# Optimization experiments

Measured on AMD Instinct MI355X. Metric: run time of the kernel, lower is better.

## Reference

```python
import math
import jax, jax.numpy as jnp
import numpy as np


def _alibi_slopes(n):
    def pow2_slopes(n):
        start = 2.0 ** (-(2.0 ** (-(math.log2(n) - 3))))
        return [start * (start ** i) for i in range(n)]
    if math.log2(n).is_integer():
        return pow2_slopes(n)
    cp2 = 2 ** math.floor(math.log2(n))
    return pow2_slopes(cp2) + _alibi_slopes(2 * cp2)[0::2][: n - cp2]


NUM_HEADS = 16


def setup_inputs() -> dict:
    key = jax.random.key(0)
    ks = jax.random.split(key, 5)
    B, S, H = 2, 2048, 2048
    return {
        "hidden_states": jax.random.normal(ks[0], (B, S, H), jnp.float32),
        "w_qkv": jax.random.normal(ks[1], (H, 3 * H), jnp.float32) * (H ** -0.5),
        "b_qkv": jax.random.normal(ks[2], (3 * H,), jnp.float32) * 0.02,
        "w_proj": jax.random.normal(ks[3], (H, H), jnp.float32) * (H ** -0.5),
        "b_proj": jax.random.normal(ks[4], (H,), jnp.float32) * 0.02,
    }


def reference(hidden_states, w_qkv, b_qkv, w_proj, b_proj):
    B, S, H = hidden_states.shape
    nh = NUM_HEADS
    hd = H // nh
    scale = 1.0 / hd  # mup scale_qk_dot_by_d=True -> d^-1 (not d^-0.5)

    qkv = hidden_states @ w_qkv + b_qkv  # [B,S,3H]
    q, k, v = jnp.split(qkv, 3, axis=-1)
    q = q.reshape(B, S, nh, hd)
    k = k.reshape(B, S, nh, hd)
    v = v.reshape(B, S, nh, hd)

    scores = jnp.einsum("bqhd,bkhd->bhqk", q, k) * scale  # [B,nh,S,S]

    slopes = jnp.asarray(_alibi_slopes(nh), dtype=scores.dtype)  # [nh]
    pos = jnp.arange(S)
    rel = (pos[None, :] - pos[:, None]).astype(scores.dtype)  # j - i, <=0 in causal region
    bias = slopes[:, None, None] * rel[None, :, :]  # [nh,S,S]
    causal = pos[None, :] <= pos[:, None]  # [S,S]

    scores = jnp.where(causal[None, None], scores + bias[None], jnp.finfo(scores.dtype).min)
    attn = jax.nn.softmax(scores, axis=-1)

    out = jnp.einsum("bhqk,bkhd->bqhd", attn, v).reshape(B, S, H)
    return out @ w_proj + b_proj
```

## Files before the change

### kernel.cpp

```cpp
#include <hip/hip_runtime.h>
#include <hip/hip_bf16.h>

typedef short bf16x8 __attribute__((ext_vector_type(8)));
typedef float f32x4 __attribute__((ext_vector_type(4)));
typedef unsigned short ushort_t;

#define NH 16
#define HD 128
#define SEQ 2048
#define HID 2048
#define NQKV 6144
#define BATCH 2

__device__ __forceinline__ ushort_t f2bf(float x) {
    unsigned u = __builtin_bit_cast(unsigned, x);
    u = (u + 0x7fffu + ((u >> 16) & 1u)) >> 16;
    return (ushort_t)u;
}

__device__ __forceinline__ void gl2lds16(const ushort_t* g, ushort_t* l) {
    __builtin_amdgcn_global_load_lds(
        (__attribute__((address_space(1))) void*)(g),
        (__attribute__((address_space(3))) void*)(l), 16, 0, 0);
}

__global__ __launch_bounds__(256) void prep_fused(
    const float* __restrict__ hidden, ushort_t* __restrict__ hbf,
    const float* __restrict__ wqkv, ushort_t* __restrict__ wqkvT,
    const float* __restrict__ wproj, ushort_t* __restrict__ wprojT) {
    const int bid = blockIdx.x;
    const int t = threadIdx.x;
    if (bid >= 12288 && bid < 16384) {
        int i = (bid - 12288) * 256 + t;
        float4 a0 = *(const float4*)(hidden + (size_t)i * 8);
        float4 a1 = *(const float4*)(hidden + (size_t)i * 8 + 4);
        union { ushort_t u[8]; uint4 v; } p;
        p.u[0]=f2bf(a0.x); p.u[1]=f2bf(a0.y); p.u[2]=f2bf(a0.z); p.u[3]=f2bf(a0.w);
        p.u[4]=f2bf(a1.x); p.u[5]=f2bf(a1.y); p.u[6]=f2bf(a1.z); p.u[7]=f2bf(a1.w);
        *(uint4*)(hbf + (size_t)i * 8) = p.v;
        return;
    }
    const float* w;
    ushort_t* wT;
    int N, bx, by;
    if (bid < 12288) {
        w = wqkv; wT = wqkvT; N = NQKV;
        bx = bid % 192; by = bid / 192;
    } else {
        int b2 = bid - 16384;
        w = wproj; wT = wprojT; N = HID;
        bx = b2 % 64; by = b2 / 64;
    }
    __shared__ float tile[32][33];
    const int nb = bx * 32, kb = by * 32;
    const int tx = t & 31, ty = t >> 5;
#pragma unroll
    for (int i = 0; i < 4; ++i) {
        int k = kb + ty + i * 8;
        tile[ty + i * 8][tx] = w[(size_t)k * N + nb + tx];
    }
    __syncthreads();
#pragma unroll
    for (int i = 0; i < 4; ++i) {
        int n = nb + ty + i * 8;
        wT[(size_t)n * HID + kb + tx] = f2bf(tile[tx][ty + i * 8]);
    }
}

#define GEMM_KLOOP(A_, BT_)                                                     \
    const int t = threadIdx.x;                                                  \
    const int w = t >> 6, lane = t & 63, lm = lane & 15, lq = lane >> 4;        \
    const int wm = (w >> 1) * 64, wn = (w & 1) * 64;                            \
    const int lrow = lane >> 3, lsw = (lane & 7) ^ lrow;                        \
    f32x4 acc[4][4] = {};                                                       \
    const ushort_t* gA = A_ + (size_t)(mb + w * 32 + lrow) * HID + lsw * 8;     \
    const ushort_t* gB = BT_ + (size_t)(nb + w * 32 + lrow) * HID + lsw * 8;    \
    for (int kb = 0; kb < HID; kb += 64) {                                      \
        __syncthreads();                                                        \
        _Pragma("unroll")                                                       \
        for (int c = 0; c < 4; ++c) {                                           \
            gl2lds16(gA + (size_t)c * 8 * HID + kb, At + (w * 256 + c * 64) * 8); \
            gl2lds16(gB + (size_t)c * 8 * HID + kb, Bt + (w * 256 + c * 64) * 8); \
        }                                                                       \
        __syncthreads();                                                        \
        _Pragma("unroll")                                                       \
        for (int kc = 0; kc < 2; ++kc) {                                        \
            const int slot = (kc * 4 + lq) ^ (lm & 7);                          \
            bf16x8 af[4], bfr[4];                                               \
            _Pragma("unroll")                                                   \
            for (int mt = 0; mt < 4; ++mt)                                      \
                af[mt] = ((const bf16x8*)At)[(wm + mt * 16 + lm) * 8 + slot];   \
            _Pragma("unroll")                                                   \
            for (int nt = 0; nt < 4; ++nt)                                      \
                bfr[nt] = ((const bf16x8*)Bt)[(wn + nt * 16 + lm) * 8 + slot];  \
            _Pragma("unroll")                                                   \
            for (int mt = 0; mt < 4; ++mt)                                      \
                _Pragma("unroll")                                               \
                for (int nt = 0; nt < 4; ++nt)                                  \
                    acc[mt][nt] = __builtin_amdgcn_mfma_f32_16x16x32_bf16(      \
                        af[mt], bfr[nt], acc[mt][nt], 0, 0, 0);                 \
        }                                                                       \
    }

__global__ __launch_bounds__(256) void gemm_qkv(
    const ushort_t* __restrict__ A, const ushort_t* __restrict__ BT,
    const float* __restrict__ bias,
    ushort_t* __restrict__ qbuf, ushort_t* __restrict__ kbuf,
    ushort_t* __restrict__ vTbuf) {
    __shared__ unsigned shbuf[128 * 68];
    ushort_t* At = (ushort_t*)shbuf;
    ushort_t* Bt = At + 128 * 64;
    const int mb = blockIdx.x * 128;
    const int nb = blockIdx.y * 128;
    GEMM_KLOOP(A, BT)

    const int sec = nb >> 11;
    if (sec < 2) {
#pragma unroll
        for (int mt = 0; mt < 4; ++mt)
#pragma unroll
            for (int nt = 0; nt < 4; ++nt)
#pragma unroll
                for (int r = 0; r < 4; ++r) {
                    int m = mb + wm + mt * 16 + lq * 4 + r;
                    int c = nb + wn + nt * 16 + lm;
                    float val = acc[mt][nt][r] + bias[c];
                    int h = (c >> 7) & 15;
                    int d = c & 127;
                    int b = m >> 11, s = m & 2047;
                    size_t bh = (size_t)(b * NH + h);
                    ushort_t* dst = (sec == 0) ? qbuf : kbuf;
                    dst[(bh * SEQ + s) * HD + d] = f2bf(val);
                }
    } else {
        __syncthreads();
        unsigned* T = shbuf;
#pragma unroll
        for (int mt = 0; mt < 4; ++mt)
#pragma unroll
            for (int nt = 0; nt < 4; ++nt) {
                const int cl = wn + nt * 16 + lm;
                const int ml = wm + mt * 16 + lq * 4;
                const float bb = bias[nb + cl];
#pragma unroll
                for (int r = 0; r < 4; r += 2) {
                    unsigned pk = (unsigned)f2bf(acc[mt][nt][r] + bb) |
                                  ((unsigned)f2bf(acc[mt][nt][r + 1] + bb) << 16);
                    T[cl * 68 + ((ml + r) >> 1)] = pk;
                }
            }
        __syncthreads();
        const int d = t & 127, sh = t >> 7;
        const int b = mb >> 11, sbase = mb & 2047;
        const int hv = (nb >> 7) - 32;
        ushort_t* vrow = vTbuf + ((size_t)(b * NH + hv) * HD + d) * SEQ + sbase + sh * 64;
#pragma unroll
        for (int i = 0; i < 8; ++i)
            *(uint4*)(vrow + i * 8) = *(const uint4*)&T[d * 68 + sh * 32 + i * 4];
    }
}

__global__ __launch_bounds__(256) void gemm_proj(
    const ushort_t* __restrict__ A, const ushort_t* __restrict__ BT,
    const float* __restrict__ bias, float* __restrict__ out) {
    __shared__ ushort_t Abuf[128 * 64];
    __shared__ ushort_t Bbuf[128 * 64];
    ushort_t* At = Abuf;
    ushort_t* Bt = Bbuf;
    const int mb = blockIdx.x * 128;
    const int nb = blockIdx.y * 128;
    GEMM_KLOOP(A, BT)
#pragma unroll
    for (int mt = 0; mt < 4; ++mt)
#pragma unroll
        for (int nt = 0; nt < 4; ++nt)
#pragma unroll
            for (int r = 0; r < 4; ++r) {
                int m = mb + wm + mt * 16 + lq * 4 + r;
                int c = nb + wn + nt * 16 + lm;
                out[(size_t)m * HID + c] = acc[mt][nt][r] + bias[c];
            }
}

__global__ __launch_bounds__(256) void attn_kernel(
    const ushort_t* __restrict__ qb, const ushort_t* __restrict__ kbuf,
    const ushort_t* __restrict__ vT, ushort_t* __restrict__ ob) {
    __shared__ ushort_t Ks[2][64 * 128];
    __shared__ ushort_t Vs[2][128 * 64];
    __shared__ ushort_t Ps[4][16 * 72];

    const int bid = blockIdx.x;
    const int x = bid & 7, g = bid >> 3;
    const int qt = 31 - (g >> 2);
    const int bh = ((g & 3) << 3) | x;
    const int qbase = qt * 64;
    const int t = threadIdx.x, w = t >> 6, lane = t & 63;
    const int lm = lane & 15, lq = lane >> 4;

    const ushort_t* Qg = qb + (size_t)bh * SEQ * HD;
    const ushort_t* Kg = kbuf + (size_t)bh * SEQ * HD;
    const ushort_t* Vg = vT + (size_t)bh * HD * SEQ;

    const float LOG2E = 1.44269504f;
    const int h = bh & 15;
    const float slope2 = exp2f(-0.5f * (float)(h + 1)) * LOG2E;
    const float scale2 = (1.0f / 128.0f) * LOG2E;

    const int qg = qbase + w * 16 + lm;

    bf16x8 qf[4];
#pragma unroll
    for (int kc = 0; kc < 4; ++kc) {
        uint4 qv = *(const uint4*)(Qg + (size_t)qg * HD + kc * 32 + lq * 8);
        qf[kc] = __builtin_bit_cast(bf16x8, qv);
    }

    float foff[4][4];
#pragma unroll
    for (int mt = 0; mt < 4; ++mt)
#pragma unroll
        for (int r = 0; r < 4; ++r)
            foff[mt][r] = slope2 * (float)(mt * 16 + lq * 4 + r);

    int koffs[4], voffs[4];
#pragma unroll
    for (int i = 0; i < 4; ++i) {
        int ci = i * 256 + t;
        int kr = ci >> 4, ks = ci & 15;
        int kcg = (ks & 8) | ((ks & 7) ^ (kr & 7));
        koffs[i] = kr * HD + kcg * 8;
        int vr = ci >> 3, vs = ci & 7;
        int vcg = vs ^ (vr & 7);
        voffs[i] = vr * SEQ + vcg * 8;
    }

#define ATTN_STAGE(KT, BUF)                                                   \
    {                                                                         \
        const ushort_t* Kt_ = Kg + (size_t)(KT) * 64 * HD;                    \
        const ushort_t* Vt_ = Vg + (size_t)(KT) * 64;                         \
        _Pragma("unroll")                                                     \
        for (int i = 0; i < 4; ++i) {                                         \
            gl2lds16(Kt_ + koffs[i], Ks[BUF] + (i * 256 + w * 64) * 8);       \
            gl2lds16(Vt_ + voffs[i], Vs[BUF] + (i * 256 + w * 64) * 8);       \
        }                                                                     \
    }

    float mrow = -1e30f, lrow = 0.0f;
    f32x4 O[8] = {};
    const int nkt = qt + 1;

    ATTN_STAGE(0, 0)
    __syncthreads();

    for (int kt = 0; kt < nkt; ++kt) {
        const int cur = kt & 1;
        if (kt + 1 < nkt) ATTN_STAGE(kt + 1, cur ^ 1)

        f32x4 sacc[4] = {};
        __builtin_amdgcn_s_setprio(1);
#pragma unroll
        for (int kc = 0; kc < 4; ++kc) {
            const int slot = ((kc * 4 + lq) & 8) | (((kc * 4 + lq) & 7) ^ (lm & 7));
#pragma unroll
            for (int mt = 0; mt < 4; ++mt) {
                bf16x8 bk = *(const bf16x8*)&Ks[cur][((mt * 16 + lm) * 16 + slot) * 8];
                sacc[mt] = __builtin_amdgcn_mfma_f32_16x16x32_bf16(bk, qf[kc], sacc[mt], 0, 0, 0);
            }
        }
        __builtin_amdgcn_s_setprio(0);

        const float sbase = slope2 * (float)(kt * 64 - qg);
        float sc[4][4];
        if (kt == qt) {
#pragma unroll
            for (int mt = 0; mt < 4; ++mt)
#pragma unroll
                for (int r = 0; r < 4; ++r) {
                    float s = sacc[mt][r] * scale2 + (sbase + foff[mt][r]);
                    sc[mt][r] = (kt * 64 + mt * 16 + lq * 4 + r <= qg) ? s : -3e38f;
                }
        } else {
#pragma unroll
            for (int mt = 0; mt < 4; ++mt)
#pragma unroll
                for (int r = 0; r < 4; ++r)
                    sc[mt][r] = sacc[mt][r] * scale2 + (sbase + foff[mt][r]);
        }

        float tm = sc[0][0];
#pragma unroll
        for (int mt = 0; mt < 4; ++mt)
#pragma unroll
            for (int r = 0; r < 4; ++r) tm = fmaxf(tm, sc[mt][r]);
        tm = fmaxf(tm, __shfl_xor(tm, 16));
        tm = fmaxf(tm, __shfl_xor(tm, 32));

        const bool noresc = __all(tm <= mrow + 8.0f) && (kt > 0);
        float mnew, alpha;
        if (noresc) {
            mnew = mrow;
            alpha = 1.0f;
        } else {
            mnew = fmaxf(mrow, tm);
            alpha = __builtin_amdgcn_exp2f(mrow - mnew);
        }
        mrow = mnew;

        float psum = 0.0f;
#pragma unroll
        for (int mt = 0; mt < 4; ++mt) {
            float p0 = __builtin_amdgcn_exp2f(sc[mt][0] - mnew);
            float p1 = __builtin_amdgcn_exp2f(sc[mt][1] - mnew);
            float p2 = __builtin_amdgcn_exp2f(sc[mt][2] - mnew);
            float p3 = __builtin_amdgcn_exp2f(sc[mt][3] - mnew);
            psum += (p0 + p1) + (p2 + p3);
            uint2 wv;
            wv.x = ((unsigned)f2bf(p1) << 16) | f2bf(p0);
            wv.y = ((unsigned)f2bf(p3) << 16) | f2bf(p2);
            *(uint2*)&Ps[w][lm * 72 + mt * 16 + lq * 4] = wv;
        }
        psum += __shfl_xor(psum, 16);
        psum += __shfl_xor(psum, 32);
        lrow = lrow * alpha + psum;

        if (!noresc) {
            float av[4];
#pragma unroll
            for (int r = 0; r < 4; ++r) av[r] = __shfl(alpha, lq * 4 + r);
#pragma unroll
            for (int nt = 0; nt < 8; ++nt)
#pragma unroll
                for (int r = 0; r < 4; ++r) O[nt][r] *= av[r];
        }

        asm volatile("s_waitcnt lgkmcnt(0)" ::: "memory");
        __builtin_amdgcn_s_setprio(1);
#pragma unroll
        for (int kc2 = 0; kc2 < 2; ++kc2) {
            bf16x8 ap = *(const bf16x8*)&Ps[w][lm * 72 + kc2 * 32 + lq * 8];
            const int slot = (kc2 * 4 + lq) ^ (lm & 7);
#pragma unroll
            for (int nt = 0; nt < 8; ++nt) {
                bf16x8 bv = *(const bf16x8*)&Vs[cur][((nt * 16 + lm) * 8 + slot) * 8];
                O[nt] = __builtin_amdgcn_mfma_f32_16x16x32_bf16(ap, bv, O[nt], 0, 0, 0);
            }
        }
        __builtin_amdgcn_s_setprio(0);

        __syncthreads();
    }

    float lb[4];
#pragma unroll
    for (int r = 0; r < 4; ++r)
        lb[r] = __builtin_amdgcn_rcpf(__shfl(lrow, lq * 4 + r));
    const int b = bh >> 4;
#pragma unroll
    for (int nt = 0; nt < 8; ++nt)
#pragma unroll
        for (int r = 0; r < 4; ++r) {
            int s = qbase + w * 16 + lq * 4 + r;
            int d = nt * 16 + lm;
            ob[((size_t)(b * SEQ + s)) * HID + h * HD + d] = f2bf(O[nt][r] * lb[r]);
        }
#undef ATTN_STAGE
}

extern "C" void kernel_launch(void* const* d_in, const int* in_sizes, int n_in,
                              void* d_out, int out_size, void* d_ws, size_t ws_size,
                              hipStream_t stream) {
    const float* hidden = (const float*)d_in[0];
    const float* w_qkv = (const float*)d_in[1];
    const float* b_qkv = (const float*)d_in[2];
    const float* w_proj = (const float*)d_in[3];
    const float* b_proj = (const float*)d_in[4];
    float* out = (float*)d_out;

    char* ws = (char*)d_ws;
    size_t off = 0;
    ushort_t* wqkvT = (ushort_t*)(ws + off); off += (size_t)NQKV * HID * 2;
    ushort_t* wprojT = (ushort_t*)(ws + off); off += (size_t)HID * HID * 2;
    ushort_t* hbf = (ushort_t*)(ws + off); off += (size_t)BATCH * SEQ * HID * 2;
    ushort_t* qw = (ushort_t*)(ws + off); off += (size_t)BATCH * NH * SEQ * HD * 2;
    ushort_t* kw = (ushort_t*)(ws + off); off += (size_t)BATCH * NH * SEQ * HD * 2;
    ushort_t* vTw = (ushort_t*)(ws + off); off += (size_t)BATCH * NH * SEQ * HD * 2;
    ushort_t* attnw = (ushort_t*)(ws + off); off += (size_t)BATCH * SEQ * HID * 2;

    prep_fused<<<dim3(20480), 256, 0, stream>>>(
        hidden, hbf, w_qkv, wqkvT, w_proj, wprojT);

    gemm_qkv<<<dim3(BATCH * SEQ / 128, NQKV / 128), 256, 0, stream>>>(
        hbf, wqkvT, b_qkv, qw, kw, vTw);

    attn_kernel<<<dim3(BATCH * NH * 32), 256, 0, stream>>>(qw, kw, vTw, attnw);

    gemm_proj<<<dim3(BATCH * SEQ / 128, HID / 128), 256, 0, stream>>>(
        attnw, wprojT, b_proj, out);
}
```

Baseline: 365.6 us.

## Rework QKV GEMM into 256x128 tiles with multi-stage LDS pipeline and enlarge attention blocks

The QKV GEMM now runs 512-thread blocks over 256x128 output tiles. It uses a hand-scheduled four-phase K loop that prefetches several half-tiles ahead into swizzled LDS, with explicit barriers, waitcnts and priority hints meant to overlap global loads with MFMA work. The attention kernel moves to 512 threads covering 128 query rows per block, so each K/V tile is shared by twice as many waves. In exchange it drops double buffering for a single buffer with two barriers per iteration, and waves past their diagonal skip compute but still join the loads and barriers. Losing load/compute overlap in attention and the idle diagonal waves could offset the gain from larger tiles.

```diff
diff --git a/kernel.cpp b/kernel.cpp
--- a/kernel.cpp
+++ b/kernel.cpp
@@ -102,61 +102,141 @@
         }                                                                       \
     }
 
-__global__ __launch_bounds__(256) void gemm_qkv(
+#define QSTAGE_A(SBUF, SKH, STILE)                                            \
+    _Pragma("unroll")                                                         \
+    for (int j = 0; j < 2; ++j)                                               \
+        gl2lds16(gA + soffA[j] + (STILE) * 64 + (SKH) * 32,                   \
+                 lds + ((SBUF) * 2 + (SKH)) * 8192 + (j * 512 + w * 64) * 8);
+
+#define QSTAGE_B(SBUF, SKH, STILE)                                            \
+    gl2lds16(gB + soffB + (STILE) * 64 + (SKH) * 32,                          \
+             lds + 32768 + ((SBUF) * 2 + (SKH)) * 4096 + (w * 64) * 8);
+
+#define QPHASE4(BUF, KH, SBUF, SKH, STILE, DRAIN)                             \
+    QSTAGE_A(SBUF, SKH, STILE)                                                \
+    QSTAGE_B(SBUF, SKH, STILE)                                                \
+    _Pragma("unroll")                                                         \
+    for (int mf = 0; mf < 4; ++mf) {                                          \
+        int rr = wm + mf * 16 + lm;                                           \
+        int slot = rr * 4 + (lq ^ ((rr >> 1) & 3));                           \
+        af[mf] = *(const bf16x8*)&lds[((BUF) * 2 + (KH)) * 8192 + slot * 8];  \
+    }                                                                         \
+    _Pragma("unroll")                                                         \
+    for (int nf = 0; nf < 4; ++nf) {                                          \
+        int rr = wn + nf * 16 + lm;                                           \
+        int slot = rr * 4 + (lq ^ ((rr >> 1) & 3));                           \
+        bfr[nf] = *(const bf16x8*)&lds[32768 + ((BUF) * 2 + (KH)) * 4096 + slot * 8]; \
+    }                                                                         \
+    asm volatile("" ::: "memory");                                            \
+    __builtin_amdgcn_s_barrier();                                             \
+    __builtin_amdgcn_sched_barrier(0);                                        \
+    __builtin_amdgcn_s_setprio(1);                                            \
+    _Pragma("unroll")                                                         \
+    for (int mf = 0; mf < 4; ++mf)                                            \
+        _Pragma("unroll")                                                     \
+        for (int nf = 0; nf < 4; ++nf)                                        \
+            acc[mf][nf] = __builtin_amdgcn_mfma_f32_16x16x32_bf16(            \
+                af[mf], bfr[nf], acc[mf][nf], 0, 0, 0);                       \
+    __builtin_amdgcn_s_setprio(0);                                            \
+    __builtin_amdgcn_sched_barrier(0);                                        \
+    if (DRAIN) { asm volatile("s_waitcnt vmcnt(3)" ::: "memory"); }           \
+    asm volatile("" ::: "memory");                                            \
+    __builtin_amdgcn_s_barrier();
+
+__global__ __launch_bounds__(512) void gemm_qkv(
     const ushort_t* __restrict__ A, const ushort_t* __restrict__ BT,
     const float* __restrict__ bias,
     ushort_t* __restrict__ qbuf, ushort_t* __restrict__ kbuf,
     ushort_t* __restrict__ vTbuf) {
-    __shared__ unsigned shbuf[128 * 68];
-    ushort_t* At = (ushort_t*)shbuf;
-    ushort_t* Bt = At + 128 * 64;
-    const int mb = blockIdx.x * 128;
-    const int nb = blockIdx.y * 128;
-    GEMM_KLOOP(A, BT)
+    __shared__ ushort_t lds[49152];
+    const int t = threadIdx.x;
+    const int w = t >> 6, lane = t & 63, lm = lane & 15, lq = lane >> 4;
+    const int wm = (w >> 1) * 64, wn = (w & 1) * 64;
+    const int mb = blockIdx.x * 256, nb = blockIdx.y * 128;
+
+    const ushort_t* gA = A + (size_t)mb * HID;
+    const ushort_t* gB = BT + (size_t)nb * HID;
+
+    int soffA[2];
+#pragma unroll
+    for (int j = 0; j < 2; ++j) {
+        int r = j * 128 + (t >> 2);
+        int c = (t & 3) ^ ((r >> 1) & 3);
+        soffA[j] = r * HID + c * 8;
+    }
+    int soffB;
+    {
+        int r = t >> 2;
+        int c = (t & 3) ^ ((r >> 1) & 3);
+        soffB = r * HID + c * 8;
+    }
+
+    f32x4 acc[4][4] = {};
+    bf16x8 af[4], bfr[4];
+
+    QSTAGE_A(0, 0, 0) QSTAGE_B(0, 0, 0)
+    QSTAGE_A(0, 1, 0) QSTAGE_B(0, 1, 0)
+    QSTAGE_A(1, 0, 1) QSTAGE_B(1, 0, 1)
+    asm volatile("s_waitcnt vmcnt(0)" ::: "memory");
+    __builtin_amdgcn_s_barrier();
+
+#pragma unroll 1
+    for (int i = 0; i < 16; ++i) {
+        const int Tb = 2 * i + 1;
+        const int T2 = (2 * i + 2) & 31, T3 = (2 * i + 3) & 31;
+        QPHASE4(0, 0, 1, 1, Tb, 0)
+        QPHASE4(0, 1, 0, 0, T2, 1)
+        QPHASE4(1, 0, 0, 1, T2, 0)
+        QPHASE4(1, 1, 1, 0, T3, 1)
+    }
+
+    asm volatile("s_waitcnt vmcnt(0)" ::: "memory");
 
     const int sec = nb >> 11;
     if (sec < 2) {
 #pragma unroll
-        for (int mt = 0; mt < 4; ++mt)
-#pragma unroll
-            for (int nt = 0; nt < 4; ++nt)
+        for (int mf = 0; mf < 4; ++mf)
+#pragma unroll
+            for (int nf = 0; nf < 4; ++nf)
 #pragma unroll
                 for (int r = 0; r < 4; ++r) {
-                    int m = mb + wm + mt * 16 + lq * 4 + r;
-                    int c = nb + wn + nt * 16 + lm;
-                    float val = acc[mt][nt][r] + bias[c];
-                    int h = (c >> 7) & 15;
+                    int m = mb + wm + mf * 16 + lq * 4 + r;
+                    int c = nb + wn + nf * 16 + lm;
+                    float val = acc[mf][nf][r] + bias[c];
+                    int hh = (c >> 7) & 15;
                     int d = c & 127;
                     int b = m >> 11, s = m & 2047;
-                    size_t bh = (size_t)(b * NH + h);
+                    size_t bh = (size_t)(b * NH + hh);
                     ushort_t* dst = (sec == 0) ? qbuf : kbuf;
                     dst[(bh * SEQ + s) * HD + d] = f2bf(val);
                 }
     } else {
         __syncthreads();
-        unsigned* T = shbuf;
-#pragma unroll
-        for (int mt = 0; mt < 4; ++mt)
-#pragma unroll
-            for (int nt = 0; nt < 4; ++nt) {
-                const int cl = wn + nt * 16 + lm;
-                const int ml = wm + mt * 16 + lq * 4;
-                const float bb = bias[nb + cl];
+        unsigned* T = (unsigned*)lds;
+        const int b = mb >> 11, sbase = mb & 2047;
+        const int hv = (nb >> 7) - 32;
+#pragma unroll
+        for (int nf = 0; nf < 4; ++nf) {
+            const int clc = wn + nf * 16 + lm;
+            const float bb = bias[nb + clc];
+#pragma unroll
+            for (int mf = 0; mf < 4; ++mf) {
+                const int ml = wm + mf * 16 + lq * 4;
 #pragma unroll
                 for (int r = 0; r < 4; r += 2) {
-                    unsigned pk = (unsigned)f2bf(acc[mt][nt][r] + bb) |
-                                  ((unsigned)f2bf(acc[mt][nt][r + 1] + bb) << 16);
-                    T[cl * 68 + ((ml + r) >> 1)] = pk;
+                    unsigned pk = (unsigned)f2bf(acc[mf][nf][r] + bb) |
+                                  ((unsigned)f2bf(acc[mf][nf][r + 1] + bb) << 16);
+                    T[clc * 132 + ((ml + r) >> 1)] = pk;
                 }
             }
+        }
         __syncthreads();
-        const int d = t & 127, sh = t >> 7;
-        const int b = mb >> 11, sbase = mb & 2047;
-        const int hv = (nb >> 7) - 32;
-        ushort_t* vrow = vTbuf + ((size_t)(b * NH + hv) * HD + d) * SEQ + sbase + sh * 64;
-#pragma unroll
-        for (int i = 0; i < 8; ++i)
-            *(uint4*)(vrow + i * 8) = *(const uint4*)&T[d * 68 + sh * 32 + i * 4];
+        const int dd = t & 127, sh = t >> 7;
+        ushort_t* vrow = vTbuf +
+            ((size_t)(b * NH + hv) * HD + dd) * SEQ + sbase + sh * 64;
+#pragma unroll
+        for (int ii = 0; ii < 8; ++ii)
+            *(uint4*)(vrow + ii * 8) = *(const uint4*)&T[dd * 132 + sh * 32 + ii * 4];
     }
 }
 
@@ -182,18 +262,18 @@
             }
 }
 
-__global__ __launch_bounds__(256) void attn_kernel(
+__global__ __launch_bounds__(512) void attn_kernel(
     const ushort_t* __restrict__ qb, const ushort_t* __restrict__ kbuf,
     const ushort_t* __restrict__ vT, ushort_t* __restrict__ ob) {
-    __shared__ ushort_t Ks[2][64 * 128];
-    __shared__ ushort_t Vs[2][128 * 64];
-    __shared__ ushort_t Ps[4][16 * 72];
+    __shared__ ushort_t Ks[64 * 128];
+    __shared__ ushort_t Vs[128 * 64];
+    __shared__ ushort_t Ps[8][16 * 72];
 
     const int bid = blockIdx.x;
     const int x = bid & 7, g = bid >> 3;
-    const int qt = 31 - (g >> 2);
+    const int qt = 15 - (g >> 2);
     const int bh = ((g & 3) << 3) | x;
-    const int qbase = qt * 64;
+    const int qbase = qt * 128;
     const int t = threadIdx.x, w = t >> 6, lane = t & 63;
     const int lm = lane & 15, lq = lane >> 4;
 
@@ -207,6 +287,7 @@
     const float scale2 = (1.0f / 128.0f) * LOG2E;
 
     const int qg = qbase + w * 16 + lm;
+    const int ktd = (qbase + w * 16) >> 6;
 
     bf16x8 qf[4];
 #pragma unroll
@@ -222,10 +303,10 @@
         for (int r = 0; r < 4; ++r)
             foff[mt][r] = slope2 * (float)(mt * 16 + lq * 4 + r);
 
-    int koffs[4], voffs[4];
-#pragma unroll
-    for (int i = 0; i < 4; ++i) {
-        int ci = i * 256 + t;
+    int koffs[2], voffs[2];
+#pragma unroll
+    for (int i = 0; i < 2; ++i) {
+        int ci = i * 512 + t;
         int kr = ci >> 4, ks = ci & 15;
         int kcg = (ks & 8) | ((ks & 7) ^ (kr & 7));
         koffs[i] = kr * HD + kcg * 8;
@@ -234,27 +315,24 @@
         voffs[i] = vr * SEQ + vcg * 8;
     }
 
-#define ATTN_STAGE(KT, BUF)                                                   \
-    {                                                                         \
-        const ushort_t* Kt_ = Kg + (size_t)(KT) * 64 * HD;                    \
-        const ushort_t* Vt_ = Vg + (size_t)(KT) * 64;                         \
-        _Pragma("unroll")                                                     \
-        for (int i = 0; i < 4; ++i) {                                         \
-            gl2lds16(Kt_ + koffs[i], Ks[BUF] + (i * 256 + w * 64) * 8);       \
-            gl2lds16(Vt_ + voffs[i], Vs[BUF] + (i * 256 + w * 64) * 8);       \
-        }                                                                     \
-    }
-
     float mrow = -1e30f, lrow = 0.0f;
     f32x4 O[8] = {};
-    const int nkt = qt + 1;
-
-    ATTN_STAGE(0, 0)
-    __syncthreads();
+    const int nkt = 2 * qt + 2;
 
     for (int kt = 0; kt < nkt; ++kt) {
-        const int cur = kt & 1;
-        if (kt + 1 < nkt) ATTN_STAGE(kt + 1, cur ^ 1)
+        __syncthreads();
+        {
+            const ushort_t* Kt_ = Kg + (size_t)kt * 64 * HD;
+            const ushort_t* Vt_ = Vg + (size_t)kt * 64;
+#pragma unroll
+            for (int i = 0; i < 2; ++i) {
+                gl2lds16(Kt_ + koffs[i], Ks + (i * 512 + w * 64) * 8);
+                gl2lds16(Vt_ + voffs[i], Vs + (i * 512 + w * 64) * 8);
+            }
+        }
+        __syncthreads();
+
+        if (kt > ktd) continue;
 
         f32x4 sacc[4] = {};
         __builtin_amdgcn_s_setprio(1);
@@ -263,7 +341,7 @@
             const int slot = ((kc * 4 + lq) & 8) | (((kc * 4 + lq) & 7) ^ (lm & 7));
 #pragma unroll
             for (int mt = 0; mt < 4; ++mt) {
-                bf16x8 bk = *(const bf16x8*)&Ks[cur][((mt * 16 + lm) * 16 + slot) * 8];
+                bf16x8 bk = *(const bf16x8*)&Ks[((mt * 16 + lm) * 16 + slot) * 8];
                 sacc[mt] = __builtin_amdgcn_mfma_f32_16x16x32_bf16(bk, qf[kc], sacc[mt], 0, 0, 0);
             }
         }
@@ -271,7 +349,7 @@
 
         const float sbase = slope2 * (float)(kt * 64 - qg);
         float sc[4][4];
-        if (kt == qt) {
+        if (kt == ktd) {
 #pragma unroll
             for (int mt = 0; mt < 4; ++mt)
 #pragma unroll
@@ -341,13 +419,11 @@
             const int slot = (kc2 * 4 + lq) ^ (lm & 7);
 #pragma unroll
             for (int nt = 0; nt < 8; ++nt) {
-                bf16x8 bv = *(const bf16x8*)&Vs[cur][((nt * 16 + lm) * 8 + slot) * 8];
+                bf16x8 bv = *(const bf16x8*)&Vs[((nt * 16 + lm) * 8 + slot) * 8];
                 O[nt] = __builtin_amdgcn_mfma_f32_16x16x32_bf16(ap, bv, O[nt], 0, 0, 0);
             }
         }
         __builtin_amdgcn_s_setprio(0);
-
-        __syncthreads();
     }
 
     float lb[4];
@@ -363,7 +439,6 @@
             int d = nt * 16 + lm;
             ob[((size_t)(b * SEQ + s)) * HID + h * HD + d] = f2bf(O[nt][r] * lb[r]);
         }
-#undef ATTN_STAGE
 }
 
 extern "C" void kernel_launch(void* const* d_in, const int* in_sizes, int n_in,
@@ -389,10 +464,10 @@
     prep_fused<<<dim3(20480), 256, 0, stream>>>(
         hidden, hbf, w_qkv, wqkvT, w_proj, wprojT);
 
-    gemm_qkv<<<dim3(BATCH * SEQ / 128, NQKV / 128), 256, 0, stream>>>(
+    gemm_qkv<<<dim3(BATCH * SEQ / 256, NQKV / 128), 512, 0, stream>>>(
         hbf, wqkvT, b_qkv, qw, kw, vTw);
 
-    attn_kernel<<<dim3(BATCH * NH * 32), 256, 0, stream>>>(qw, kw, vTw, attnw);
+    attn_kernel<<<dim3(BATCH * NH * 16), 512, 0, stream>>>(qw, kw, vTw, attnw);
 
     gemm_proj<<<dim3(BATCH * SEQ / 128, HID / 128), 256, 0, stream>>>(
         attnw, wprojT, b_proj, out);
```

Result: no change. 365.0 us (-0.2%).
